# Performance work log

Hardware: AMD Instinct MI355X
Metric: run time of the kernel (lower is better)

Reference implementation:

```python
import jax, jax.numpy as jnp
import numpy as np

GAMMA = 1.0

def setup_inputs() -> dict:
    key = jax.random.key(0)
    k1, k2 = jax.random.split(key)
    source_features = jax.random.normal(k1, (4096, 2048), dtype=jnp.float32)
    target_features = jax.random.normal(k2, (4096, 2048), dtype=jnp.float32)
    return {"source_features": source_features, "target_features": target_features}

def _gaussian_kernel_mean(x, y, gamma):
    # Original: ((x_i - y_j)**2).mean(-1) / D  == sqdist_ij / D**2
    # Computed via the x^2 + y^2 - 2xy GEMM trick instead of tiling O(N*M*D).
    d = x.shape[1]
    x2 = jnp.sum(x * x, axis=1)  # [N]
    y2 = jnp.sum(y * y, axis=1)  # [M]
    xy = x @ y.T                 # [N, M]
    sqdist = x2[:, None] + y2[None, :] - 2.0 * xy
    k = jnp.exp(-gamma * sqdist / (d * d))
    return jnp.mean(k)

def reference(source_features, target_features):
    source = source_features.reshape(source_features.shape[0], -1)
    target = target_features.reshape(target_features.shape[0], -1)
    # Equal batch sizes -> padding branch in the original is a no-op.
    xx = _gaussian_kernel_mean(source, source, GAMMA)
    yy = _gaussian_kernel_mean(target, target, GAMMA)
    xy = _gaussian_kernel_mean(source, target, GAMMA)
    return xx + yy - 2.0 * xy
```

## Files before the change

kernel.cpp:

```cpp
#include <hip/hip_runtime.h>
#include <stdint.h>
#include <stddef.h>

#define AS1 __attribute__((address_space(1)))
#define AS3 __attribute__((address_space(3)))

typedef short bf16x8 __attribute__((ext_vector_type(8)));
typedef float f32x4 __attribute__((ext_vector_type(4)));
typedef unsigned short u16x8 __attribute__((ext_vector_type(8)));

static constexpr int N = 4096;
static constexpr int K = 2048;
static constexpr int BM = 128;
static constexpr int TILES = N / BM;
static constexpr int NBLK = TILES * TILES;

__device__ __forceinline__ unsigned short f2bf(float f) {
  union { float f; uint32_t u; } v; v.f = f;
  return (unsigned short)((v.u + 0x7FFFu + ((v.u >> 16) & 1u)) >> 16);
}

__global__ __launch_bounds__(256) void prep_kernel(
    const float* __restrict__ X, const float* __restrict__ Y,
    float* __restrict__ x2, float* __restrict__ y2,
    unsigned short* __restrict__ Xb, unsigned short* __restrict__ Yb, int wb) {
  const int row = blockIdx.x;
  const float* src = blockIdx.y ? Y : X;
  float* nrm = blockIdx.y ? y2 : x2;
  unsigned short* dst = blockIdx.y ? Yb : Xb;
  const size_t base = (size_t)row * K + threadIdx.x * 8;
  const float4 a = *(const float4*)(src + base);
  const float4 b = *(const float4*)(src + base + 4);
  double s = (double)a.x * a.x + (double)a.y * a.y + (double)a.z * a.z +
             (double)a.w * a.w + (double)b.x * b.x + (double)b.y * b.y +
             (double)b.z * b.z + (double)b.w * b.w;
  if (wb) {
    u16x8 o;
    o[0] = f2bf(a.x); o[1] = f2bf(a.y); o[2] = f2bf(a.z); o[3] = f2bf(a.w);
    o[4] = f2bf(b.x); o[5] = f2bf(b.y); o[6] = f2bf(b.z); o[7] = f2bf(b.w);
    *(u16x8*)(dst + base) = o;
  }
#pragma unroll
  for (int off = 32; off; off >>= 1) s += __shfl_down(s, off);
  __shared__ double red[4];
  if ((threadIdx.x & 63) == 0) red[threadIdx.x >> 6] = s;
  __syncthreads();
  if (threadIdx.x == 0) nrm[row] = (float)(red[0] + red[1] + red[2] + red[3]);
}


#define RB(bb, o, ks) ((unsigned)((bb)*32768u + (o)*16384u + (ks)*8192u))
#define VM10 asm volatile("s_waitcnt vmcnt(10)" ::: "memory")
#define VM_NONE

#define STAGE(O, KS, TT, BB)                                                   \
  do {                                                                         \
    const unsigned short* _sp = (O) ? Bpan : Apan;                             \
    const unsigned int _kof = (unsigned)(TT) * 64u + (KS) * 32u;               \
    const unsigned int _lb = RB(BB, O, KS) + wseg;                             \
    __builtin_amdgcn_global_load_lds(                                          \
        (const AS1 unsigned int*)(_sp + ((O) ? sB0 : sA0) + _kof),             \
        (AS3 unsigned int*)(lds + _lb), 16, 0, 0);                             \
    __builtin_amdgcn_global_load_lds(                                          \
        (const AS1 unsigned int*)(_sp + ((O) ? sB1 : sA1) + _kof),             \
        (AS3 unsigned int*)(lds + _lb + 512u), 16, 0, 0);                      \
  } while (0)

#define PHASE(KS, NH, BB, VMW, ...)                                            \
  do {                                                                         \
    if constexpr ((NH) == 0) {                                                 \
      _Pragma("unroll") for (int _mi = 0; _mi < 8; ++_mi)                      \
          af[_mi] = *(const bf16x8*)(lds + RB(BB, 0, KS) + aoff[_mi]);         \
    }                                                                          \
    bf16x8 _b0 = *(const bf16x8*)(lds + RB(BB, 1, KS) + boff[(NH) * 2]);       \
    bf16x8 _b1 = *(const bf16x8*)(lds + RB(BB, 1, KS) + boff[(NH) * 2 + 1]);   \
    __VA_ARGS__;                                                               \
    __builtin_amdgcn_s_barrier();                                              \
    __builtin_amdgcn_s_setprio(1);                                             \
    _Pragma("unroll") for (int _mi = 0; _mi < 8; ++_mi) {                      \
      acc[_mi][(NH) * 2] = __builtin_amdgcn_mfma_f32_16x16x32_bf16(            \
          af[_mi], _b0, acc[_mi][(NH) * 2], 0, 0, 0);                          \
      acc[_mi][(NH) * 2 + 1] = __builtin_amdgcn_mfma_f32_16x16x32_bf16(        \
          af[_mi], _b1, acc[_mi][(NH) * 2 + 1], 0, 0, 0);                      \
    }                                                                          \
    __builtin_amdgcn_s_setprio(0);                                             \
    VMW;                                                                       \
    __builtin_amdgcn_s_barrier();                                              \
  } while (0)

#define TILE(T, BB)                                                            \
  do {                                                                         \
    const int _t1 = ((T) + 1 < 32) ? (T) + 1 : 31;                             \
    const int _t2 = ((T) + 2 < 32) ? (T) + 2 : 31;                             \
    PHASE(0, 0, BB, VM_NONE, STAGE(1, 1, _t1, 1 - (BB)));                      \
    PHASE(0, 1, BB, VM10, STAGE(0, 0, _t2, BB));                               \
    PHASE(1, 0, BB, VM_NONE, STAGE(1, 0, _t2, BB));                            \
    PHASE(1, 1, BB, VM10, STAGE(0, 1, _t2, BB));                               \
  } while (0)

__global__ __launch_bounds__(512, 2) void mmd_gemm8(
    const unsigned short* __restrict__ Xb, const unsigned short* __restrict__ Yb,
    const float* __restrict__ x2, const float* __restrict__ y2,
    double* __restrict__ partials) {
  __shared__ __align__(16) unsigned short lds[65536];

  const int bid = blockIdx.x;
  const int logical = (bid & 7) * 32 + (bid >> 3);
  const int i0 = (logical & 15) << 8;
  const int j0 = (logical >> 4) << 8;

  const unsigned short* Apan = Xb;
  const unsigned short* Bpan = Yb;
  const float* rn = x2;
  const float* cn = y2;

  const int tid = threadIdx.x;
  const int w = tid >> 6, l = tid & 63;
  const int wm = w >> 2, wn = w & 3;
  const int lr = l & 15, lq = l >> 4;

  const int ci0 = w * 128 + l;
  const int ci1 = ci0 + 64;
  const int r0 = ci0 >> 2, r1 = ci1 >> 2;
  const int c0 = ((ci0 & 3) - (r0 >> 2)) & 3;
  const int c1 = ((ci1 & 3) - (r1 >> 2)) & 3;
  const unsigned int sA0 = (unsigned)(i0 + r0) * (unsigned)K + (unsigned)(c0 * 8);
  const unsigned int sA1 = (unsigned)(i0 + r1) * (unsigned)K + (unsigned)(c1 * 8);
  const unsigned int sB0 = (unsigned)(j0 + r0) * (unsigned)K + (unsigned)(c0 * 8);
  const unsigned int sB1 = (unsigned)(j0 + r1) * (unsigned)K + (unsigned)(c1 * 8);
  const unsigned int wseg = (unsigned)w * 1024u;

  unsigned int aoff[8], boff[4];
#pragma unroll
  for (int mi = 0; mi < 8; ++mi) {
    const int r = wm * 128 + mi * 16 + lr;
    aoff[mi] = (unsigned)(r * 32 + (((lq + (r >> 2)) & 3) * 8));
  }
#pragma unroll
  for (int ni = 0; ni < 4; ++ni) {
    const int rb = wn * 64 + ni * 16 + lr;
    boff[ni] = (unsigned)(rb * 32 + (((lq + (rb >> 2)) & 3) * 8));
  }

  f32x4 acc[8][4] = {};
  bf16x8 af[8];

  STAGE(0, 0, 0, 0); STAGE(1, 0, 0, 0); STAGE(0, 1, 0, 0); STAGE(1, 1, 0, 0);
  STAGE(0, 0, 1, 1); STAGE(1, 0, 1, 1); STAGE(0, 1, 1, 1);
  VM10;
  __builtin_amdgcn_s_barrier();

#pragma unroll 1
  for (int tt = 0; tt < 32; tt += 2) {
    TILE(tt, 0);
    TILE(tt + 1, 1);
  }

  const float ce = -1.0f / (2048.0f * 2048.0f);
  double s = 0.0;
#pragma unroll
  for (int mi = 0; mi < 8; ++mi) {
#pragma unroll
    for (int r4 = 0; r4 < 4; ++r4) {
      const float rv = rn[i0 + wm * 128 + mi * 16 + lq * 4 + r4];
#pragma unroll
      for (int ni = 0; ni < 4; ++ni) {
        const float cv = cn[j0 + wn * 64 + ni * 16 + lr];
        const float tx = ce * (rv + cv - 2.0f * acc[mi][ni][r4]);
        const float v =
            tx * (1.0f + tx * (0.5f + tx * (0.16666667f + tx * 0.041666668f)));
        s += (double)v;
      }
    }
  }
#pragma unroll
  for (int off = 32; off; off >>= 1) s += __shfl_down(s, off);
  __shared__ double red[8];
  if (l == 0) red[w] = s;
  __syncthreads();
  if (tid == 0) {
    double tot = 0.0;
#pragma unroll
    for (int i = 0; i < 8; ++i) tot += red[i];
    partials[logical] = -2.0 * tot;
  }
}

__global__ __launch_bounds__(256) void mmd_sym128(
    const unsigned short* __restrict__ Xb, const unsigned short* __restrict__ Yb,
    const float* __restrict__ x2, const float* __restrict__ y2,
    double* __restrict__ partials) {
  const int bid = blockIdx.x;
  const int logical = (bid & 7) * 132 + (bid >> 3);
  const int p = (logical >= 528) ? 1 : 0;
  int jj = logical - (p ? 528 : 0);
  int rr = 0;
  while (jj >= 32 - rr) { jj -= 32 - rr; ++rr; }
  const int ti = rr, tj = rr + jj;
  const double wgt = (ti == tj) ? 1.0 : 2.0;

  const unsigned short* Pan = p ? Yb : Xb;
  const float* nrm = p ? y2 : x2;
  const int i0 = ti * 128, j0 = tj * 128;

  __shared__ __align__(16) unsigned short As[128 * 64];
  __shared__ __align__(16) unsigned short Bs[128 * 64];

  const int tid = threadIdx.x;
  const int w = tid >> 6, l = tid & 63;
  const int m_base = (w >> 1) * 64, n_base = (w & 1) * 64;
  const int lr = l & 15, lq = l >> 4;

  f32x4 acc[4][4] = {};

  for (int k0 = 0; k0 < K; k0 += 64) {
#pragma unroll
    for (int u = 0; u < 4; ++u) {
      const int seg = w * 4 + u;
      const int f = seg * 64 + l;
      const int row = f >> 3;
      const int scol = ((f & 7) ^ (row & 7)) * 8;
      __builtin_amdgcn_global_load_lds(
          (const AS1 unsigned int*)(Pan + (size_t)(i0 + row) * K + k0 + scol),
          (AS3 unsigned int*)(As + seg * 512), 16, 0, 0);
      __builtin_amdgcn_global_load_lds(
          (const AS1 unsigned int*)(Pan + (size_t)(j0 + row) * K + k0 + scol),
          (AS3 unsigned int*)(Bs + seg * 512), 16, 0, 0);
    }
    __syncthreads();

#pragma unroll
    for (int kk = 0; kk < 64; kk += 32) {
      bf16x8 af2[4], bfr[4];
      const int ch = (kk >> 3) + lq;
#pragma unroll
      for (int mi = 0; mi < 4; ++mi) {
        const int r = m_base + mi * 16 + lr;
        af2[mi] = *(const bf16x8*)((const char*)As + r * 128 + ((ch ^ (r & 7)) * 16));
      }
#pragma unroll
      for (int ni = 0; ni < 4; ++ni) {
        const int r = n_base + ni * 16 + lr;
        bfr[ni] = *(const bf16x8*)((const char*)Bs + r * 128 + ((ch ^ (r & 7)) * 16));
      }
#pragma unroll
      for (int mi = 0; mi < 4; ++mi)
#pragma unroll
        for (int ni = 0; ni < 4; ++ni)
          acc[mi][ni] = __builtin_amdgcn_mfma_f32_16x16x32_bf16(
              af2[mi], bfr[ni], acc[mi][ni], 0, 0, 0);
    }
    __syncthreads();
  }

  const float ce = -1.0f / (2048.0f * 2048.0f);
  double s = 0.0;
#pragma unroll
  for (int mi = 0; mi < 4; ++mi) {
#pragma unroll
    for (int r4 = 0; r4 < 4; ++r4) {
      const float rv = nrm[i0 + m_base + mi * 16 + lq * 4 + r4];
#pragma unroll
      for (int ni = 0; ni < 4; ++ni) {
        const float cv = nrm[j0 + n_base + ni * 16 + lr];
        const float tx = ce * (rv + cv - 2.0f * acc[mi][ni][r4]);
        const float v =
            tx * (1.0f + tx * (0.5f + tx * (0.16666667f + tx * 0.041666668f)));
        s += (double)v;
      }
    }
  }
#pragma unroll
  for (int off = 32; off; off >>= 1) s += __shfl_down(s, off);
  __shared__ double red[4];
  if (l == 0) red[w] = s;
  __syncthreads();
  if (tid == 0)
    partials[256 + logical] = wgt * (red[0] + red[1] + red[2] + red[3]);
}

__global__ __launch_bounds__(256) void mmd_gemm_f32(
    const float* __restrict__ Xp, const float* __restrict__ Yp,
    const float* __restrict__ x2, const float* __restrict__ y2,
    double* __restrict__ partials) {
  const int p = blockIdx.y;
  const float* Ap = (p == 1) ? Yp : Xp;
  const float* Bp = (p == 0) ? Xp : Yp;
  const float* rn = (p == 1) ? y2 : x2;
  const float* cn = (p == 0) ? x2 : y2;
  const double wgt = (p == 2) ? -2.0 : 1.0;

  const int bx = blockIdx.x;
  const int i0 = (bx & (TILES - 1)) * BM;
  const int j0 = (bx / TILES) * BM;

  __shared__ __align__(16) unsigned short As[BM * 64];
  __shared__ __align__(16) unsigned short Bs[BM * 64];

  const int tid = threadIdx.x;
  const int w = tid >> 6, l = tid & 63;
  const int m_base = (w >> 1) * 64, n_base = (w & 1) * 64;

  f32x4 acc[4][4] = {};

  for (int k0 = 0; k0 < K; k0 += 64) {
#pragma unroll
    for (int u = 0; u < 4; ++u) {
      const int f = u * 256 + tid;
      const int row = f >> 3;
      const int cir = f & 7;
      const int dstb = row * 128 + ((cir ^ (row & 7)) * 16);
      {
        const float* g = Ap + (size_t)(i0 + row) * K + k0 + cir * 8;
        const float4 v0 = *(const float4*)g;
        const float4 v1 = *(const float4*)(g + 4);
        u16x8 o;
        o[0] = f2bf(v0.x); o[1] = f2bf(v0.y); o[2] = f2bf(v0.z); o[3] = f2bf(v0.w);
        o[4] = f2bf(v1.x); o[5] = f2bf(v1.y); o[6] = f2bf(v1.z); o[7] = f2bf(v1.w);
        *(u16x8*)((char*)As + dstb) = o;
      }
      {
        const float* g = Bp + (size_t)(j0 + row) * K + k0 + cir * 8;
        const float4 v0 = *(const float4*)g;
        const float4 v1 = *(const float4*)(g + 4);
        u16x8 o;
        o[0] = f2bf(v0.x); o[1] = f2bf(v0.y); o[2] = f2bf(v0.z); o[3] = f2bf(v0.w);
        o[4] = f2bf(v1.x); o[5] = f2bf(v1.y); o[6] = f2bf(v1.z); o[7] = f2bf(v1.w);
        *(u16x8*)((char*)Bs + dstb) = o;
      }
    }
    __syncthreads();

#pragma unroll
    for (int kk = 0; kk < 64; kk += 32) {
      bf16x8 af2[4], bfr[4];
      const int lr = l & 15;
      const int ch = (kk >> 3) + (l >> 4);
#pragma unroll
      for (int mi = 0; mi < 4; ++mi) {
        const int r = m_base + mi * 16 + lr;
        af2[mi] = *(const bf16x8*)((const char*)As + r * 128 + ((ch ^ (r & 7)) * 16));
      }
#pragma unroll
      for (int ni = 0; ni < 4; ++ni) {
        const int r = n_base + ni * 16 + lr;
        bfr[ni] = *(const bf16x8*)((const char*)Bs + r * 128 + ((ch ^ (r & 7)) * 16));
      }
#pragma unroll
      for (int mi = 0; mi < 4; ++mi)
#pragma unroll
        for (int ni = 0; ni < 4; ++ni)
          acc[mi][ni] = __builtin_amdgcn_mfma_f32_16x16x32_bf16(
              af2[mi], bfr[ni], acc[mi][ni], 0, 0, 0);
    }
    __syncthreads();
  }

  const float ce = -1.0f / (2048.0f * 2048.0f);
  double s = 0.0;
  const int lr = l & 15, lq = l >> 4;
#pragma unroll
  for (int mi = 0; mi < 4; ++mi) {
#pragma unroll
    for (int r4 = 0; r4 < 4; ++r4) {
      const float rv = rn[i0 + m_base + mi * 16 + lq * 4 + r4];
#pragma unroll
      for (int ni = 0; ni < 4; ++ni) {
        const float cv = cn[j0 + n_base + ni * 16 + lr];
        const float tx = ce * (rv + cv - 2.0f * acc[mi][ni][r4]);
        const float v =
            tx * (1.0f + tx * (0.5f + tx * (0.16666667f + tx * 0.041666668f)));
        s += (double)v;
      }
    }
  }
#pragma unroll
  for (int off = 32; off; off >>= 1) s += __shfl_down(s, off);
  __shared__ double red[4];
  if (l == 0) red[w] = s;
  __syncthreads();
  if (tid == 0) partials[p * NBLK + bx] = wgt * (red[0] + red[1] + red[2] + red[3]);
}

__global__ __launch_bounds__(256) void finalize_kernel(
    const double* __restrict__ partials, float* __restrict__ out, int n) {
  double s = 0.0;
  for (int i = threadIdx.x; i < n; i += 256) s += partials[i];
#pragma unroll
  for (int off = 32; off; off >>= 1) s += __shfl_down(s, off);
  __shared__ double red[4];
  if ((threadIdx.x & 63) == 0) red[threadIdx.x >> 6] = s;
  __syncthreads();
  if (threadIdx.x == 0)
    out[0] = (float)((red[0] + red[1] + red[2] + red[3]) *
                     (1.0 / ((double)N * (double)N)));
}

extern "C" void kernel_launch(void* const* d_in, const int* in_sizes, int n_in,
                              void* d_out, int out_size, void* d_ws,
                              size_t ws_size, hipStream_t stream) {
  const float* X = (const float*)d_in[0];
  const float* Y = (const float*)d_in[1];
  char* ws = (char*)d_ws;

  double* partials = (double*)ws;
  float* x2 = (float*)(ws + 24576);
  float* y2 = (float*)(ws + 24576 + 16384);
  unsigned short* Xb = (unsigned short*)(ws + 65536);
  unsigned short* Yb = Xb + (size_t)N * K;
  const size_t need_fast = (size_t)65536 + (size_t)2 * N * K * 2;
  const bool fast = ws_size >= need_fast;

  prep_kernel<<<dim3(N, 2), 256, 0, stream>>>(X, Y, x2, y2, Xb, Yb, fast ? 1 : 0);
  if (fast) {
    mmd_gemm8<<<dim3(256), dim3(512), 0, stream>>>(Xb, Yb, x2, y2, partials);
    mmd_sym128<<<dim3(1056), dim3(256), 0, stream>>>(Xb, Yb, x2, y2, partials);
    finalize_kernel<<<1, 256, 0, stream>>>(partials, (float*)d_out, 1312);
  } else {
    mmd_gemm_f32<<<dim3(NBLK, 3), 256, 0, stream>>>(X, Y, x2, y2, partials);
    finalize_kernel<<<1, 256, 0, stream>>>(partials, (float*)d_out, 3072);
  }
}
```

Baseline: 198.2 us.

## Route off-diagonal symmetric tiles through the fast 256x256 GEMM kernel

```diff
diff --git a/kernel.cpp b/kernel.cpp
--- a/kernel.cpp
+++ b/kernel.cpp
@@ -105,14 +105,26 @@
   __shared__ __align__(16) unsigned short lds[65536];
 
   const int bid = blockIdx.x;
-  const int logical = (bid & 7) * 32 + (bid >> 3);
-  const int i0 = (logical & 15) << 8;
-  const int j0 = (logical >> 4) << 8;
-
-  const unsigned short* Apan = Xb;
-  const unsigned short* Bpan = Yb;
-  const float* rn = x2;
-  const float* cn = y2;
+  const int logical = (bid & 7) * 62 + (bid >> 3);
+  int ti, tj;
+  const unsigned short *Apan, *Bpan;
+  const float *rn, *cn;
+  double wgt;
+  if (logical < 256) {
+    ti = logical & 15; tj = logical >> 4;
+    Apan = Xb; Bpan = Yb; rn = x2; cn = y2; wgt = -2.0;
+  } else {
+    const int q = logical - 256;
+    const int pp = q / 120;
+    int jj = q % 120;
+    int rr = 0;
+    while (jj >= 15 - rr) { jj -= 15 - rr; ++rr; }
+    ti = rr; tj = rr + 1 + jj;
+    Apan = Bpan = pp ? Yb : Xb;
+    rn = cn = pp ? y2 : x2;
+    wgt = 2.0;
+  }
+  const int i0 = ti << 8, j0 = tj << 8;
 
   const int tid = threadIdx.x;
   const int w = tid >> 6, l = tid & 63;
@@ -182,7 +194,7 @@
     double tot = 0.0;
 #pragma unroll
     for (int i = 0; i < 8; ++i) tot += red[i];
-    partials[logical] = -2.0 * tot;
+    partials[logical] = wgt * tot;
   }
 }
 
@@ -191,17 +203,17 @@
     const float* __restrict__ x2, const float* __restrict__ y2,
     double* __restrict__ partials) {
   const int bid = blockIdx.x;
-  const int logical = (bid & 7) * 132 + (bid >> 3);
-  const int p = (logical >= 528) ? 1 : 0;
-  int jj = logical - (p ? 528 : 0);
-  int rr = 0;
-  while (jj >= 32 - rr) { jj -= 32 - rr; ++rr; }
-  const int ti = rr, tj = rr + jj;
-  const double wgt = (ti == tj) ? 1.0 : 2.0;
+  const int logical = (bid & 7) * 12 + (bid >> 3);
+  const int p = logical / 48;
+  const int r2_ = logical % 48;
+  const int d = r2_ / 3;
+  const int sub = r2_ % 3;
+  const double wgt = (sub == 1) ? 2.0 : 1.0;
 
   const unsigned short* Pan = p ? Yb : Xb;
   const float* nrm = p ? y2 : x2;
-  const int i0 = ti * 128, j0 = tj * 128;
+  const int i0 = d * 256 + ((sub == 2) ? 128 : 0);
+  const int j0 = d * 256 + ((sub >= 1) ? 128 : 0);
 
   __shared__ __align__(16) unsigned short As[128 * 64];
   __shared__ __align__(16) unsigned short Bs[128 * 64];
@@ -276,7 +288,7 @@
   if (l == 0) red[w] = s;
   __syncthreads();
   if (tid == 0)
-    partials[256 + logical] = wgt * (red[0] + red[1] + red[2] + red[3]);
+    partials[496 + logical] = wgt * (red[0] + red[1] + red[2] + red[3]);
 }
 
 __global__ __launch_bounds__(256) void mmd_gemm_f32(
@@ -413,9 +425,9 @@
 
   prep_kernel<<<dim3(N, 2), 256, 0, stream>>>(X, Y, x2, y2, Xb, Yb, fast ? 1 : 0);
   if (fast) {
-    mmd_gemm8<<<dim3(256), dim3(512), 0, stream>>>(Xb, Yb, x2, y2, partials);
-    mmd_sym128<<<dim3(1056), dim3(256), 0, stream>>>(Xb, Yb, x2, y2, partials);
-    finalize_kernel<<<1, 256, 0, stream>>>(partials, (float*)d_out, 1312);
+    mmd_gemm8<<<dim3(496), dim3(512), 0, stream>>>(Xb, Yb, x2, y2, partials);
+    mmd_sym128<<<dim3(96), dim3(256), 0, stream>>>(Xb, Yb, x2, y2, partials);
+    finalize_kernel<<<1, 256, 0, stream>>>(partials, (float*)d_out, 592);
   } else {
     mmd_gemm_f32<<<dim3(NBLK, 3), 256, 0, stream>>>(X, Y, x2, y2, partials);
     finalize_kernel<<<1, 256, 0, stream>>>(partials, (float*)d_out, 3072);
```

After: 183.0 us. 1.08x faster.
